# Kernel tuning notes

Hardware: AMD Instinct MI355X
Metric: run time of the kernel (lower is better)

The kernel has to match this reference:

```python
import jax, jax.numpy as jnp
import numpy as np
from jax import lax

B, H, W = 16, 64, 64
CHANNELS = 512
N_BLOCKS, CIN_B, COUT_B = 16, 32, 32
K = 3  # kernel size, 'same' padding, stride 1


def setup_inputs() -> dict:
    key = jax.random.key(0)
    k1, k2, k3, k4, k5 = jax.random.split(key, 5)
    x = jax.random.normal(k1, (B, H, W, CHANNELS), dtype=jnp.float32)
    # per-block conv kernels, HWIO per block: [n_blocks, kh, kw, cin_b, cout_b]
    fan_in = K * K * CIN_B
    weights = jax.random.normal(k2, (N_BLOCKS, K, K, CIN_B, COUT_B), dtype=jnp.float32) / np.sqrt(fan_in)
    bias = jax.random.normal(k3, (CHANNELS,), dtype=jnp.float32) * 0.05
    # disjoint channel partitions (realistic block routing); gather may duplicate, scatter sums
    blocks_in = jax.random.permutation(k4, CHANNELS).reshape(N_BLOCKS, CIN_B).astype(jnp.int32)
    blocks_out = jax.random.permutation(k5, CHANNELS).reshape(N_BLOCKS, COUT_B).astype(jnp.int32)
    return {"x": x, "weights": weights, "bias": bias,
            "blocks_in": blocks_in, "blocks_out": blocks_out}


def reference(x, weights, bias, blocks_in, blocks_out):
    n_blocks, cin_b = blocks_in.shape
    cout_b = blocks_out.shape[1]
    # gather: [B,H,W, n_blocks*cin_b], grouped channel layout
    xg = x[..., blocks_in.reshape(-1)]
    # grouped-conv kernel HWIO: I=cin_b per group, O = n_blocks*cout_b (groups along O)
    kernel = jnp.transpose(weights, (1, 2, 3, 0, 4)).reshape(K, K, cin_b, n_blocks * cout_b)
    y = lax.conv_general_dilated(
        xg, kernel, window_strides=(1, 1), padding='SAME',
        dimension_numbers=('NHWC', 'HWIO', 'NHWC'),
        feature_group_count=n_blocks)  # [B,H,W, n_blocks*cout_b]
    # scatter_nd semantics: duplicates accumulate
    out = jnp.zeros((x.shape[0], y.shape[1], y.shape[2], CHANNELS), dtype=y.dtype)
    out = out.at[..., blocks_out.reshape(-1)].add(y)
    out = out + bias
    return jax.nn.relu(out)
```

## Files before the change

kernel.cpp:

```cpp
#include <hip/hip_runtime.h>

#define B_ 16
#define H_ 64
#define W_ 64
#define C_ 512
#define NG 16

#define WT 16
#define SEG 16

#define SLOT_BYTES (18*512*2)
#define XS_BYTES   (3*SLOT_BYTES)
#define OROW_OFF   XS_BYTES
#define OROW_BYTES (16*512*4)
#define POS_OFF    (OROW_OFF + OROW_BYTES)
#define SMEM_BYTES (POS_OFF + 512*2)

typedef __attribute__((ext_vector_type(8))) short bf16x8;
typedef __attribute__((ext_vector_type(4))) float f32x4;

__device__ __forceinline__ short f2bf(float f) {
  union { float f; unsigned u; } v; v.f = f;
  unsigned r = v.u + 0x7FFFu + ((v.u >> 16) & 1u);
  return (short)(r >> 16);
}

__global__ __launch_bounds__(1024, 4) void bconv_kernel(
    const float* __restrict__ x, const float* __restrict__ wts,
    const float* __restrict__ bias, const int* __restrict__ bin,
    const int* __restrict__ bout, float* __restrict__ out)
{
  extern __shared__ char smem[];
  unsigned short* pos_tab = (unsigned short*)(smem + POS_OFF);
  float* orow = (float*)(smem + OROW_OFF);

  const int t    = threadIdx.x;
  const int lane = t & 63;
  const int g    = t >> 6;
  const int g4   = lane >> 4;
  const int n16  = lane & 15;

  const int bid   = blockIdx.x;
  const int b     = bid >> 4;
  const int strip = (bid >> 2) & 3;
  const int seg   = bid & 3;
  const int hs = seg * SEG;
  const int w0 = strip * WT;

  if (t < 512) pos_tab[bin[t]] = (unsigned short)t;

  bf16x8 wf[9][2];
  {
    const float* Wg = wts + g * (9*32*32);
#pragma unroll
    for (int tap = 0; tap < 9; ++tap) {
#pragma unroll
      for (int nt = 0; nt < 2; ++nt) {
        bf16x8 f;
#pragma unroll
        for (int j = 0; j < 8; ++j)
          f[j] = f2bf(Wg[(tap*32 + g4*8 + j)*32 + nt*16 + n16]);
        wf[tap][nt] = f;
      }
    }
  }

  const int opos0 = bout[g*32 + n16];
  const int opos1 = bout[g*32 + 16 + n16];

  const int c4   = (t & 127) << 2;
  const int pixq = t >> 7;
  const f32x4 bias4 = *(const f32x4*)(bias + c4);

  __syncthreads();

  unsigned pk[3][2];
  int go[3];
#pragma unroll
  for (int s = 0; s < 3; ++s) {
    int v = t + s*1024;
    if (v < 2304) {
      int col = v >> 7;
      int cc4 = (v & 127) << 2;
      unsigned sw = (unsigned)((col & 7) << 4);
      unsigned o0 = ((unsigned)((col*512 + pos_tab[cc4+0])*2)) ^ sw;
      unsigned o1 = ((unsigned)((col*512 + pos_tab[cc4+1])*2)) ^ sw;
      unsigned o2 = ((unsigned)((col*512 + pos_tab[cc4+2])*2)) ^ sw;
      unsigned o3 = ((unsigned)((col*512 + pos_tab[cc4+3])*2)) ^ sw;
      pk[s][0] = o0 | (o1 << 16);
      pk[s][1] = o2 | (o3 << 16);
      int gcol = w0 - 1 + col;
      go[s] = (gcol >= 0 && gcol < W_) ? ((gcol*512 + cc4) * 4) : -1;
    } else {
      go[s] = -2;
    }
  }

  for (int pr = 0; pr < 3; ++pr) {
    int grow = hs - 1 + pr;
    char* sb = smem + ((grow + 3) % 3) * SLOT_BYTES;
    const char* xrow = (const char*)(x + (size_t)(b*H_ + (grow < 0 ? 0 : grow)) * W_ * C_);
    bool rv = (grow >= 0) && (grow < H_);
#pragma unroll
    for (int s = 0; s < 3; ++s) {
      if (go[s] == -2) continue;
      f32x4 r = {0.f,0.f,0.f,0.f};
      if (rv && go[s] >= 0) r = *(const f32x4*)(xrow + go[s]);
      unsigned p0 = pk[s][0], p1 = pk[s][1];
      *(short*)(sb + (p0 & 0xFFFFu)) = f2bf(r[0]);
      *(short*)(sb + (p0 >> 16))     = f2bf(r[1]);
      *(short*)(sb + (p1 & 0xFFFFu)) = f2bf(r[2]);
      *(short*)(sb + (p1 >> 16))     = f2bf(r[3]);
    }
  }
  __syncthreads();

  const int gbase = g*64 + g4*16;
  const size_t outb_base = (size_t)b * H_ * W_ * C_;

  for (int h = hs; h < hs + SEG; ++h) {
    const int grow = h + 2;
    const bool want = (h <= hs + SEG - 2);
    f32x4 r0 = {0.f,0.f,0.f,0.f}, r1 = {0.f,0.f,0.f,0.f}, r2 = {0.f,0.f,0.f,0.f};
    {
      const char* xrow = (const char*)(x + (size_t)(b*H_ + (grow < H_ ? grow : 0)) * W_ * C_);
      bool rv = want && (grow < H_);
      if (rv && go[0] >= 0) r0 = *(const f32x4*)(xrow + go[0]);
      if (rv && go[1] >= 0) r1 = *(const f32x4*)(xrow + go[1]);
      if (go[2] != -2 && rv && go[2] >= 0) r2 = *(const f32x4*)(xrow + go[2]);
    }

    f32x4 a0 = {0.f,0.f,0.f,0.f}, a1 = {0.f,0.f,0.f,0.f};
#pragma unroll
    for (int dh = 0; dh < 3; ++dh) {
      const char* sb = smem + ((h - 1 + dh + 3) % 3) * SLOT_BYTES;
#pragma unroll
      for (int dw = 0; dw < 3; ++dw) {
        int col = n16 + dw;
        int addr = (col*1024 + gbase) ^ ((col & 7) << 4);
        bf16x8 a = *(const bf16x8*)(sb + addr);
        a0 = __builtin_amdgcn_mfma_f32_16x16x32_bf16(a, wf[dh*3+dw][0], a0, 0, 0, 0);
        a1 = __builtin_amdgcn_mfma_f32_16x16x32_bf16(a, wf[dh*3+dw][1], a1, 0, 0, 0);
      }
    }
    __syncthreads();

#pragma unroll
    for (int rr = 0; rr < 4; ++rr) {
      int m = (g4*4 + rr) * 512;
      orow[m + opos0] = a0[rr];
      orow[m + opos1] = a1[rr];
    }
    if (want) {
      char* sb = smem + (grow % 3) * SLOT_BYTES;
      if (go[0] != -2) {
        unsigned p0 = pk[0][0], p1 = pk[0][1];
        *(short*)(sb + (p0 & 0xFFFFu)) = f2bf(r0[0]);
        *(short*)(sb + (p0 >> 16))     = f2bf(r0[1]);
        *(short*)(sb + (p1 & 0xFFFFu)) = f2bf(r0[2]);
        *(short*)(sb + (p1 >> 16))     = f2bf(r0[3]);
      }
      if (go[1] != -2) {
        unsigned p0 = pk[1][0], p1 = pk[1][1];
        *(short*)(sb + (p0 & 0xFFFFu)) = f2bf(r1[0]);
        *(short*)(sb + (p0 >> 16))     = f2bf(r1[1]);
        *(short*)(sb + (p1 & 0xFFFFu)) = f2bf(r1[2]);
        *(short*)(sb + (p1 >> 16))     = f2bf(r1[3]);
      }
      if (go[2] != -2) {
        unsigned p0 = pk[2][0], p1 = pk[2][1];
        *(short*)(sb + (p0 & 0xFFFFu)) = f2bf(r2[0]);
        *(short*)(sb + (p0 >> 16))     = f2bf(r2[1]);
        *(short*)(sb + (p1 & 0xFFFFu)) = f2bf(r2[2]);
        *(short*)(sb + (p1 >> 16))     = f2bf(r2[3]);
      }
    }
    __syncthreads();

#pragma unroll
    for (int s = 0; s < 2; ++s) {
      int pix = pixq + s*8;
      f32x4 y = *(const f32x4*)(orow + pix*512 + c4);
      f32x4 o;
      o[0] = fmaxf(y[0] + bias4[0], 0.f);
      o[1] = fmaxf(y[1] + bias4[1], 0.f);
      o[2] = fmaxf(y[2] + bias4[2], 0.f);
      o[3] = fmaxf(y[3] + bias4[3], 0.f);
      *(f32x4*)(out + outb_base + (size_t)(h*W_ + w0 + pix) * C_ + c4) = o;
    }
  }
}

extern "C" void kernel_launch(void* const* d_in, const int* in_sizes, int n_in,
                              void* d_out, int out_size, void* d_ws, size_t ws_size,
                              hipStream_t stream) {
  const float* x    = (const float*)d_in[0];
  const float* wts  = (const float*)d_in[1];
  const float* bias = (const float*)d_in[2];
  const int*   bin  = (const int*)d_in[3];
  const int*   bout = (const int*)d_in[4];
  float* out = (float*)d_out;
  (void)in_sizes; (void)n_in; (void)out_size; (void)d_ws; (void)ws_size;

  bconv_kernel<<<dim3(256), dim3(1024), SMEM_BYTES, stream>>>(x, wts, bias, bin, bout, out);
}
```

Before: 110.2 us.

## Split gather into pre-permute bf16 kernel and stream rows via global_load_lds

Adds a separate permute kernel that gathers input channels into grouped order, converts them to bf16 and swizzles them into a workspace buffer. The conv kernel then stages rows with direct global-to-LDS loads into a 4-slot ring, and double-buffers the output row so the epilogue store overlaps the next row's compute with one barrier per row. This removes the per-thread scattered LDS writes and halves the bytes the conv reads per halo row. In exchange it adds a second launch plus a workspace write and read round trip.

Measured after the change: 131.5 us. +19.4%, slower.

```diff
diff --git a/kernel.cpp b/kernel.cpp
--- a/kernel.cpp
+++ b/kernel.cpp
@@ -1,23 +1,13 @@
 #include <hip/hip_runtime.h>
 
-#define B_ 16
-#define H_ 64
-#define W_ 64
-#define C_ 512
-#define NG 16
-
-#define WT 16
-#define SEG 16
-
-#define SLOT_BYTES (18*512*2)
-#define XS_BYTES   (3*SLOT_BYTES)
-#define OROW_OFF   XS_BYTES
-#define OROW_BYTES (16*512*4)
-#define POS_OFF    (OROW_OFF + OROW_BYTES)
-#define SMEM_BYTES (POS_OFF + 512*2)
+#define NSLOT 4
+#define SLOT_B 18432
+#define OROW_OFF (NSLOT*SLOT_B)
+#define SMEM2 (OROW_OFF + 2*16*512*4)
 
 typedef __attribute__((ext_vector_type(8))) short bf16x8;
 typedef __attribute__((ext_vector_type(4))) float f32x4;
+typedef __attribute__((ext_vector_type(4))) unsigned int u32x4;
 
 __device__ __forceinline__ short f2bf(float f) {
   union { float f; unsigned u; } v; v.f = f;
@@ -25,168 +15,175 @@
   return (short)(r >> 16);
 }
 
-__global__ __launch_bounds__(1024, 4) void bconv_kernel(
-    const float* __restrict__ x, const float* __restrict__ wts,
-    const float* __restrict__ bias, const int* __restrict__ bin,
-    const int* __restrict__ bout, float* __restrict__ out)
+__device__ __forceinline__ void gld_lds16(const void* g, void* l) {
+  __builtin_amdgcn_global_load_lds(
+      (__attribute__((address_space(1))) void*)(g),
+      (__attribute__((address_space(3))) void*)(l), 16, 0, 0);
+}
+
+__global__ __launch_bounds__(256) void permute_kernel(
+    const float* __restrict__ x, const int* __restrict__ bin,
+    unsigned char* __restrict__ xs)
+{
+  __shared__ unsigned short pos_tab[512];
+  __shared__ char stage[4][1024];
+  const int t = threadIdx.x;
+  { int c0 = bin[t], c1 = bin[t + 256];
+    pos_tab[c0] = (unsigned short)t; pos_tab[c1] = (unsigned short)(t + 256); }
+  __syncthreads();
+
+  const int w = t >> 6, lane = t & 63;
+  char* st = stage[w];
+  const int pbase = blockIdx.x * 32 + w * 8;
+  for (int i = 0; i < 8; ++i) {
+    const int p = pbase + i;
+    const unsigned swz = (unsigned)((((p & 63) + 1) & 7) << 4);
+    const float* src = x + (size_t)p * 512 + lane * 4;
+    f32x4 v0 = *(const f32x4*)(src);
+    f32x4 v1 = *(const f32x4*)(src + 256);
+    const int cb = lane * 4;
+#pragma unroll
+    for (int k = 0; k < 4; ++k)
+      *(short*)(st + (((unsigned)pos_tab[cb + k] * 2u) ^ swz)) = f2bf(v0[k]);
+#pragma unroll
+    for (int k = 0; k < 4; ++k)
+      *(short*)(st + (((unsigned)pos_tab[256 + cb + k] * 2u) ^ swz)) = f2bf(v1[k]);
+    asm volatile("s_waitcnt lgkmcnt(0)" ::: "memory");
+    u32x4 d = *(const u32x4*)(st + lane * 16);
+    *(u32x4*)(xs + (size_t)p * 1024 + lane * 16) = d;
+  }
+}
+
+__global__ __launch_bounds__(1024, 4) void conv_kernel(
+    const unsigned char* __restrict__ xs, const float* __restrict__ wts,
+    const float* __restrict__ bias, const int* __restrict__ bout,
+    float* __restrict__ out)
 {
   extern __shared__ char smem[];
-  unsigned short* pos_tab = (unsigned short*)(smem + POS_OFF);
   float* orow = (float*)(smem + OROW_OFF);
 
-  const int t    = threadIdx.x;
+  const int t = threadIdx.x;
   const int lane = t & 63;
-  const int g    = t >> 6;
-  const int g4   = lane >> 4;
-  const int n16  = lane & 15;
-
-  const int bid   = blockIdx.x;
-  const int b     = bid >> 4;
+  const int g = t >> 6;
+  const int g4 = lane >> 4;
+  const int n16 = lane & 15;
+
+  const int bid = blockIdx.x;
+  const int b = bid >> 4;
   const int strip = (bid >> 2) & 3;
-  const int seg   = bid & 3;
-  const int hs = seg * SEG;
-  const int w0 = strip * WT;
-
-  if (t < 512) pos_tab[bin[t]] = (unsigned short)t;
+  const int seg = bid & 3;
+  const int hs = seg * 16;
+  const int w0 = strip * 16;
+
+  {
+    u32x4 z = {0, 0, 0, 0};
+    for (int zz = t; zz < (NSLOT * SLOT_B) / 16; zz += 1024)
+      *(u32x4*)(smem + zz * 16) = z;
+  }
 
   bf16x8 wf[9][2];
   {
-    const float* Wg = wts + g * (9*32*32);
-#pragma unroll
-    for (int tap = 0; tap < 9; ++tap) {
+    const float* Wg = wts + g * (9 * 32 * 32);
+#pragma unroll
+    for (int tap = 0; tap < 9; ++tap)
 #pragma unroll
       for (int nt = 0; nt < 2; ++nt) {
         bf16x8 f;
 #pragma unroll
         for (int j = 0; j < 8; ++j)
-          f[j] = f2bf(Wg[(tap*32 + g4*8 + j)*32 + nt*16 + n16]);
+          f[j] = f2bf(Wg[(tap * 32 + g4 * 8 + j) * 32 + nt * 16 + n16]);
         wf[tap][nt] = f;
       }
-    }
-  }
-
-  const int opos0 = bout[g*32 + n16];
-  const int opos1 = bout[g*32 + 16 + n16];
-
-  const int c4   = (t & 127) << 2;
+  }
+  const int opos0 = bout[g * 32 + n16];
+  const int opos1 = bout[g * 32 + 16 + n16];
+  const int c4 = (t & 127) << 2;
   const int pixq = t >> 7;
   const f32x4 bias4 = *(const f32x4*)(bias + c4);
 
+  auto stage_row = [&](int grow) {
+    if (grow < 0 || grow > 63) return;
+    char* slot = smem + (grow & 3) * SLOT_B;
+    const unsigned char* src = xs + ((size_t)((b * 64 + grow) * 64 + (w0 - 1)) * 1024);
+    int gcol0 = w0 - 1 + g;
+    if (gcol0 >= 0)
+      gld_lds16(src + g * 1024 + lane * 16, slot + g * 1024);
+    if (g < 2) {
+      int c = g + 16;
+      if (w0 - 1 + c < 64)
+        gld_lds16(src + c * 1024 + lane * 16, slot + c * 1024);
+    }
+  };
+
   __syncthreads();
-
-  unsigned pk[3][2];
-  int go[3];
-#pragma unroll
-  for (int s = 0; s < 3; ++s) {
-    int v = t + s*1024;
-    if (v < 2304) {
-      int col = v >> 7;
-      int cc4 = (v & 127) << 2;
-      unsigned sw = (unsigned)((col & 7) << 4);
-      unsigned o0 = ((unsigned)((col*512 + pos_tab[cc4+0])*2)) ^ sw;
-      unsigned o1 = ((unsigned)((col*512 + pos_tab[cc4+1])*2)) ^ sw;
-      unsigned o2 = ((unsigned)((col*512 + pos_tab[cc4+2])*2)) ^ sw;
-      unsigned o3 = ((unsigned)((col*512 + pos_tab[cc4+3])*2)) ^ sw;
-      pk[s][0] = o0 | (o1 << 16);
-      pk[s][1] = o2 | (o3 << 16);
-      int gcol = w0 - 1 + col;
-      go[s] = (gcol >= 0 && gcol < W_) ? ((gcol*512 + cc4) * 4) : -1;
-    } else {
-      go[s] = -2;
-    }
-  }
-
-  for (int pr = 0; pr < 3; ++pr) {
-    int grow = hs - 1 + pr;
-    char* sb = smem + ((grow + 3) % 3) * SLOT_BYTES;
-    const char* xrow = (const char*)(x + (size_t)(b*H_ + (grow < 0 ? 0 : grow)) * W_ * C_);
-    bool rv = (grow >= 0) && (grow < H_);
-#pragma unroll
-    for (int s = 0; s < 3; ++s) {
-      if (go[s] == -2) continue;
-      f32x4 r = {0.f,0.f,0.f,0.f};
-      if (rv && go[s] >= 0) r = *(const f32x4*)(xrow + go[s]);
-      unsigned p0 = pk[s][0], p1 = pk[s][1];
-      *(short*)(sb + (p0 & 0xFFFFu)) = f2bf(r[0]);
-      *(short*)(sb + (p0 >> 16))     = f2bf(r[1]);
-      *(short*)(sb + (p1 & 0xFFFFu)) = f2bf(r[2]);
-      *(short*)(sb + (p1 >> 16))     = f2bf(r[3]);
-    }
-  }
+  stage_row(hs - 1); stage_row(hs); stage_row(hs + 1);
   __syncthreads();
 
-  const int gbase = g*64 + g4*16;
-  const size_t outb_base = (size_t)b * H_ * W_ * C_;
-
-  for (int h = hs; h < hs + SEG; ++h) {
-    const int grow = h + 2;
-    const bool want = (h <= hs + SEG - 2);
-    f32x4 r0 = {0.f,0.f,0.f,0.f}, r1 = {0.f,0.f,0.f,0.f}, r2 = {0.f,0.f,0.f,0.f};
-    {
-      const char* xrow = (const char*)(x + (size_t)(b*H_ + (grow < H_ ? grow : 0)) * W_ * C_);
-      bool rv = want && (grow < H_);
-      if (rv && go[0] >= 0) r0 = *(const f32x4*)(xrow + go[0]);
-      if (rv && go[1] >= 0) r1 = *(const f32x4*)(xrow + go[1]);
-      if (go[2] != -2 && rv && go[2] >= 0) r2 = *(const f32x4*)(xrow + go[2]);
-    }
-
-    f32x4 a0 = {0.f,0.f,0.f,0.f}, a1 = {0.f,0.f,0.f,0.f};
+  const int gbase = g * 64 + g4 * 16;
+  const size_t outb = (size_t)b * (64 * 64 * 512);
+  const int hstage_max = (hs + 16 < 63) ? hs + 16 : 63;
+
+  for (int h = hs; h < hs + 16; ++h) {
+    if (h + 2 <= hstage_max) {
+      stage_row(h + 2);
+    } else if (h + 2 == 64) {
+      u32x4 z = {0, 0, 0, 0};
+      *(u32x4*)(smem + t * 16) = z;
+      if (t < 128) *(u32x4*)(smem + 16384 + t * 16) = z;
+    }
+
+    if (h > hs) {
+      const float* ob = orow + ((h - 1) & 1) * 8192;
+#pragma unroll
+      for (int s = 0; s < 2; ++s) {
+        int pix = pixq + s * 8;
+        f32x4 y = *(const f32x4*)(ob + pix * 512 + c4);
+        f32x4 o;
+        o[0] = fmaxf(y[0] + bias4[0], 0.f);
+        o[1] = fmaxf(y[1] + bias4[1], 0.f);
+        o[2] = fmaxf(y[2] + bias4[2], 0.f);
+        o[3] = fmaxf(y[3] + bias4[3], 0.f);
+        *(f32x4*)(out + outb + (size_t)((h - 1) * 64 + w0 + pix) * 512 + c4) = o;
+      }
+    }
+
+    f32x4 a0 = {0, 0, 0, 0}, a1 = {0, 0, 0, 0};
 #pragma unroll
     for (int dh = 0; dh < 3; ++dh) {
-      const char* sb = smem + ((h - 1 + dh + 3) % 3) * SLOT_BYTES;
+      const char* sb = smem + ((h - 1 + dh) & 3) * SLOT_B;
 #pragma unroll
       for (int dw = 0; dw < 3; ++dw) {
         int col = n16 + dw;
-        int addr = (col*1024 + gbase) ^ ((col & 7) << 4);
+        int addr = (col * 1024 + gbase) ^ ((col & 7) << 4);
         bf16x8 a = *(const bf16x8*)(sb + addr);
-        a0 = __builtin_amdgcn_mfma_f32_16x16x32_bf16(a, wf[dh*3+dw][0], a0, 0, 0, 0);
-        a1 = __builtin_amdgcn_mfma_f32_16x16x32_bf16(a, wf[dh*3+dw][1], a1, 0, 0, 0);
+        a0 = __builtin_amdgcn_mfma_f32_16x16x32_bf16(a, wf[dh * 3 + dw][0], a0, 0, 0, 0);
+        a1 = __builtin_amdgcn_mfma_f32_16x16x32_bf16(a, wf[dh * 3 + dw][1], a1, 0, 0, 0);
       }
     }
+
+    float* oh = orow + (h & 1) * 8192;
+#pragma unroll
+    for (int rr = 0; rr < 4; ++rr) {
+      int m = (g4 * 4 + rr) * 512;
+      oh[m + opos0] = a0[rr];
+      oh[m + opos1] = a1[rr];
+    }
     __syncthreads();
-
-#pragma unroll
-    for (int rr = 0; rr < 4; ++rr) {
-      int m = (g4*4 + rr) * 512;
-      orow[m + opos0] = a0[rr];
-      orow[m + opos1] = a1[rr];
-    }
-    if (want) {
-      char* sb = smem + (grow % 3) * SLOT_BYTES;
-      if (go[0] != -2) {
-        unsigned p0 = pk[0][0], p1 = pk[0][1];
-        *(short*)(sb + (p0 & 0xFFFFu)) = f2bf(r0[0]);
-        *(short*)(sb + (p0 >> 16))     = f2bf(r0[1]);
-        *(short*)(sb + (p1 & 0xFFFFu)) = f2bf(r0[2]);
-        *(short*)(sb + (p1 >> 16))     = f2bf(r0[3]);
-      }
-      if (go[1] != -2) {
-        unsigned p0 = pk[1][0], p1 = pk[1][1];
-        *(short*)(sb + (p0 & 0xFFFFu)) = f2bf(r1[0]);
-        *(short*)(sb + (p0 >> 16))     = f2bf(r1[1]);
-        *(short*)(sb + (p1 & 0xFFFFu)) = f2bf(r1[2]);
-        *(short*)(sb + (p1 >> 16))     = f2bf(r1[3]);
-      }
-      if (go[2] != -2) {
-        unsigned p0 = pk[2][0], p1 = pk[2][1];
-        *(short*)(sb + (p0 & 0xFFFFu)) = f2bf(r2[0]);
-        *(short*)(sb + (p0 >> 16))     = f2bf(r2[1]);
-        *(short*)(sb + (p1 & 0xFFFFu)) = f2bf(r2[2]);
-        *(short*)(sb + (p1 >> 16))     = f2bf(r2[3]);
-      }
-    }
-    __syncthreads();
-
+  }
+
+  {
+    const int h1 = hs + 15;
+    const float* ob = orow + (h1 & 1) * 8192;
 #pragma unroll
     for (int s = 0; s < 2; ++s) {
-      int pix = pixq + s*8;
-      f32x4 y = *(const f32x4*)(orow + pix*512 + c4);
+      int pix = pixq + s * 8;
+      f32x4 y = *(const f32x4*)(ob + pix * 512 + c4);
       f32x4 o;
       o[0] = fmaxf(y[0] + bias4[0], 0.f);
       o[1] = fmaxf(y[1] + bias4[1], 0.f);
       o[2] = fmaxf(y[2] + bias4[2], 0.f);
       o[3] = fmaxf(y[3] + bias4[3], 0.f);
-      *(f32x4*)(out + outb_base + (size_t)(h*W_ + w0 + pix) * C_ + c4) = o;
+      *(f32x4*)(out + outb + (size_t)(h1 * 64 + w0 + pix) * 512 + c4) = o;
     }
   }
 }
@@ -200,7 +197,9 @@
   const int*   bin  = (const int*)d_in[3];
   const int*   bout = (const int*)d_in[4];
   float* out = (float*)d_out;
-  (void)in_sizes; (void)n_in; (void)out_size; (void)d_ws; (void)ws_size;
-
-  bconv_kernel<<<dim3(256), dim3(1024), SMEM_BYTES, stream>>>(x, wts, bias, bin, bout, out);
-}
+  unsigned char* xs = (unsigned char*)d_ws;
+  (void)in_sizes; (void)n_in; (void)out_size; (void)ws_size;
+
+  permute_kernel<<<dim3(2048), dim3(256), 0, stream>>>(x, bin, xs);
+  conv_kernel<<<dim3(256), dim3(1024), SMEM2, stream>>>(xs, wts, bias, bout, out);
+}
```
